# Performance work log

Hardware: AMD Instinct MI355X
Metric: run time of the kernel (lower is better)

## Reference

```python
import jax, jax.numpy as jnp
import numpy as np
import math

N_EMBD = 1024
N_HEAD = 16
N_CTX = 2048
SCALE = True
NEG = 1e10


def setup_inputs() -> dict:
    key = jax.random.key(0)
    ks = jax.random.split(key, 4)
    B, S = 2, 2048
    x = jax.random.normal(ks[0], (B, S, N_EMBD), dtype=jnp.float32)
    c_attn_w = jax.random.normal(ks[1], (N_EMBD, 3 * N_EMBD), dtype=jnp.float32) * 0.02
    c_attn_b = jnp.zeros((3 * N_EMBD,), dtype=jnp.float32)
    c_proj_w = jax.random.normal(ks[2], (N_EMBD, N_EMBD), dtype=jnp.float32) * 0.02
    c_proj_b = jnp.zeros((N_EMBD,), dtype=jnp.float32)
    return {"x": x, "c_attn_w": c_attn_w, "c_attn_b": c_attn_b,
            "c_proj_w": c_proj_w, "c_proj_b": c_proj_b}


def reference(x, c_attn_w, c_attn_b, c_proj_w, c_proj_b):
    B, S, D = x.shape
    H = N_HEAD
    hd = D // H
    qkv = x @ c_attn_w + c_attn_b                      # [B,S,3D]
    q, k, v = jnp.split(qkv, 3, axis=-1)
    # split heads -> [B,H,S,hd]
    q = q.reshape(B, S, H, hd).transpose(0, 2, 1, 3)
    k = k.reshape(B, S, H, hd).transpose(0, 2, 1, 3)
    v = v.reshape(B, S, H, hd).transpose(0, 2, 1, 3)
    w = jnp.einsum('bhqd,bhkd->bhqk', q, k)           # [B,H,S,S]
    if SCALE:
        w = w / math.sqrt(hd)
    # multiplicative causal mask trick: w*b - 1e10*(1-b)
    b = jnp.tril(jnp.ones((S, S), dtype=w.dtype))[None, None]
    w = w * b - NEG * (1.0 - b)
    w = jax.nn.softmax(w, axis=-1)
    a = jnp.einsum('bhqk,bhkd->bhqd', w, v)           # [B,H,S,hd]
    a = a.transpose(0, 2, 1, 3).reshape(B, S, D)      # merge heads
    a = a @ c_proj_w + c_proj_b
    present = jnp.stack((k, v))                       # [2,B,H,S,hd]
    return a, present
```

## Files before the change

### kernel.cpp

```cpp
#include <hip/hip_runtime.h>
#include <hip/hip_bf16.h>
#include <cstdint>
#include <cstddef>

#define SEQ 2048
#define DMODEL 1024
#define NHEAD 16
#define HDIM 64
#define MTOT 4096
#define NQKV 3072
#define KDIM 1024

#define OUT_K_BASE  4194304u
#define OUT_V_BASE  8388608u

#define QSCALE 0.18033688011112043f

typedef __attribute__((ext_vector_type(4))) float f32x4;
typedef __attribute__((ext_vector_type(8))) __bf16 bf16x8;
typedef __attribute__((ext_vector_type(8))) short s16x8;
typedef __attribute__((ext_vector_type(4))) short s16x4;
typedef __attribute__((ext_vector_type(2))) int i32x2;

static __device__ __forceinline__ unsigned short f2bf(float f) {
  unsigned int u = __builtin_bit_cast(unsigned int, f);
  u += 0x7FFFu + ((u >> 16) & 1u);
  return (unsigned short)(u >> 16);
}

static __device__ __forceinline__ float bf2f(unsigned short u) {
  unsigned int x = ((unsigned int)u) << 16;
  return __builtin_bit_cast(float, x);
}

static __device__ __forceinline__ s16x4 pack4(float4 v) {
  s16x4 r;
  r[0] = (short)f2bf(v.x);
  r[1] = (short)f2bf(v.y);
  r[2] = (short)f2bf(v.z);
  r[3] = (short)f2bf(v.w);
  return r;
}

static __device__ __forceinline__ int cvtpk(float lo, float hi) {
  int r;
  asm("v_cvt_pk_bf16_f32 %0, %1, %2" : "=v"(r) : "v"(lo), "v"(hi));
  return r;
}

static __device__ __forceinline__ f32x4 mfma16(s16x8 a, s16x8 b, f32x4 c) {
  return __builtin_amdgcn_mfma_f32_16x16x32_bf16(
      __builtin_bit_cast(bf16x8, a), __builtin_bit_cast(bf16x8, b), c, 0, 0, 0);
}

static __device__ __forceinline__ void gload16(const void* g, void* l) {
  __builtin_amdgcn_global_load_lds(
      (const __attribute__((address_space(1))) unsigned int*)(uintptr_t)g,
      (__attribute__((address_space(3))) unsigned int*)(uintptr_t)l,
      16, 0, 0);
}

#define WAITVM(n) asm volatile("s_waitcnt vmcnt(" #n ")" ::: "memory")

__global__ __launch_bounds__(256) void convert_x(
    const float* __restrict__ X, unsigned short* __restrict__ Xbf)
{
  int i = blockIdx.x * 256 + threadIdx.x;
  float4 v = reinterpret_cast<const float4*>(X)[i];
  reinterpret_cast<s16x4*>(Xbf)[i] = pack4(v);
}

__global__ __launch_bounds__(256) void convert_wt(
    const float* __restrict__ W, unsigned short* __restrict__ Wt, int N)
{
  __shared__ unsigned short t[64][72];
  const int n0 = blockIdx.x * 64, k0 = blockIdx.y * 64;
  const int tid = threadIdx.x;
#pragma unroll
  for (int i = 0; i < 4; ++i) {
    int f = tid + (i << 8);
    int r = f >> 4, c4 = (f & 15) << 2;
    float4 v = *reinterpret_cast<const float4*>(&W[(size_t)(k0 + r) * N + n0 + c4]);
    *reinterpret_cast<s16x4*>(&t[r][c4]) = pack4(v);
  }
  __syncthreads();
#pragma unroll
  for (int i = 0; i < 2; ++i) {
    int g = tid + (i << 8);
    int n = g >> 3, k8 = (g & 7) << 3;
    s16x8 o;
#pragma unroll
    for (int jj = 0; jj < 8; ++jj) o[jj] = (short)t[k8 + jj][n];
    *reinterpret_cast<s16x8*>(&Wt[(size_t)(n0 + n) * KDIM + k0 + k8]) = o;
  }
}

__global__ __launch_bounds__(256) void qkv_gemm(
    const unsigned short* __restrict__ Xbf,
    const unsigned short* __restrict__ Wt,
    const float* __restrict__ Bias,
    unsigned short* __restrict__ Qbf,
    unsigned short* __restrict__ Kbf,
    unsigned short* __restrict__ Vt,
    float* __restrict__ outp)
{
  __shared__ __align__(16) unsigned short lds_a[2][128][64];
  __shared__ __align__(16) unsigned short lds_b[2][128][64];

  const int tid = threadIdx.x;
  const int lane = tid & 63;
  const int wv = tid >> 6;
  const int wr = wv >> 1, wc = wv & 1;
  const int m0 = blockIdx.x * 128;
  const int n0 = blockIdx.y * 128;
  const int lr = lane & 15;
  const int gq = lane >> 4;

  const f32x4 fzero = {0.f, 0.f, 0.f, 0.f};
  f32x4 acc[4][4];
#pragma unroll
  for (int i = 0; i < 4; ++i)
#pragma unroll
    for (int j = 0; j < 4; ++j) acc[i][j] = fzero;

  {
    const int r0 = tid >> 3;
    const int c0 = tid & 7;
    auto stage = [&](int nb, int kk) {
#pragma unroll
      for (int i = 0; i < 4; ++i) {
        int r = r0 + (i << 5);
        int sc = ((c0 ^ (r & 7)) << 3);
        int ub = (((i << 8) + (wv << 6)) << 3);
        gload16(&Xbf[(size_t)(m0 + r) * KDIM + kk + sc], &lds_a[nb][0][0] + ub);
        gload16(&Wt[(size_t)(n0 + r) * KDIM + kk + sc], &lds_b[nb][0][0] + ub);
      }
    };
    stage(0, 0);
    stage(1, 64);
    for (int t = 0; t < 16; ++t) {
      if (t < 15) { WAITVM(8); } else { WAITVM(0); }
      __builtin_amdgcn_s_barrier();
      const int bufg = t & 1;
      __builtin_amdgcn_s_setprio(1);
#pragma unroll
      for (int kf = 0; kf < 2; ++kf) {
        s16x8 bfv[4];
#pragma unroll
        for (int ni = 0; ni < 4; ++ni) {
          int row = wc * 64 + ni * 16 + lr;
          bfv[ni] = *reinterpret_cast<const s16x8*>(
              &lds_b[bufg][row][((kf * 4 + gq) ^ (row & 7)) << 3]);
        }
#pragma unroll
        for (int mi = 0; mi < 4; ++mi) {
          int row = wr * 64 + mi * 16 + lr;
          s16x8 af = *reinterpret_cast<const s16x8*>(
              &lds_a[bufg][row][((kf * 4 + gq) ^ (row & 7)) << 3]);
#pragma unroll
          for (int ni = 0; ni < 4; ++ni)
            acc[mi][ni] = mfma16(af, bfv[ni], acc[mi][ni]);
        }
      }
      __builtin_amdgcn_s_setprio(0);
      __builtin_amdgcn_s_barrier();
      if (t < 14) stage(bufg, (t + 2) << 6);
    }
  }

  __syncthreads();
  unsigned short* T = (wv < 2) ? (&lds_a[0][0][0] + (wv << 12))
                               : (&lds_b[0][0][0] + ((wv - 2) << 12));
  const int seg = n0 >> 10;
  const int b = m0 >> 11;
  const int s0 = (m0 & 2047) + wr * 64;
  const int h = ((n0 & 1023) >> 6) + wc;
  const size_t bh = (size_t)(b * NHEAD + h);

  if (seg <= 1) {
#pragma unroll
    for (int ni = 0; ni < 4; ++ni) {
      int c = n0 + wc * 64 + ni * 16 + lr;
      float bias = Bias[c];
      int ch = 2 * ni + (lr >> 3);
      int el = lr & 7;
#pragma unroll
      for (int mi = 0; mi < 4; ++mi)
#pragma unroll
        for (int j = 0; j < 4; ++j) {
          int s_loc = mi * 16 + gq * 4 + j;
          float val = acc[mi][ni][j] + bias;
          if (seg == 0) val *= QSCALE;
          T[s_loc * 64 + ((ch ^ (s_loc & 7)) << 3) + el] = f2bf(val);
        }
    }
    unsigned short* dst = (seg == 0) ? Qbf : Kbf;
#pragma unroll
    for (int it = 0; it < 8; ++it) {
      int rr = (lane >> 3) + (it << 3);
      int cl = lane & 7;
      s16x8 vv = *reinterpret_cast<const s16x8*>(
          &T[rr * 64 + ((cl ^ (rr & 7)) << 3)]);
      size_t off = (bh * SEQ + s0 + rr) * HDIM + (cl << 3);
      *reinterpret_cast<s16x8*>(&dst[off]) = vv;
      if (seg == 1) {
        float4 lo = {bf2f((unsigned short)vv[0]), bf2f((unsigned short)vv[1]),
                     bf2f((unsigned short)vv[2]), bf2f((unsigned short)vv[3])};
        float4 hi = {bf2f((unsigned short)vv[4]), bf2f((unsigned short)vv[5]),
                     bf2f((unsigned short)vv[6]), bf2f((unsigned short)vv[7])};
        *reinterpret_cast<float4*>(&outp[OUT_K_BASE + off]) = lo;
        *reinterpret_cast<float4*>(&outp[OUT_K_BASE + off + 4]) = hi;
      }
    }
  } else {
#pragma unroll
    for (int ni = 0; ni < 4; ++ni) {
      int c = n0 + wc * 64 + ni * 16 + lr;
      float bias = Bias[c];
      int d_loc = ni * 16 + lr;
      int dsw = d_loc & 7;
#pragma unroll
      for (int mi = 0; mi < 4; ++mi)
#pragma unroll
        for (int j = 0; j < 4; ++j) {
          int s_loc = mi * 16 + gq * 4 + j;
          T[d_loc * 64 + (((s_loc >> 3) ^ dsw) << 3) + (s_loc & 7)] =
              f2bf(acc[mi][ni][j] + bias);
        }
    }
#pragma unroll
    for (int it = 0; it < 8; ++it) {
      int dl = (lane >> 3) + (it << 3);
      int cl = lane & 7;
      s16x8 vv = *reinterpret_cast<const s16x8*>(
          &T[dl * 64 + ((cl ^ (dl & 7)) << 3)]);
      *reinterpret_cast<s16x8*>(
          &Vt[(bh * HDIM + dl) * SEQ + s0 + (cl << 3)]) = vv;
    }
#pragma unroll
    for (int ni = 0; ni < 4; ++ni) {
      int c = n0 + wc * 64 + ni * 16 + lr;
      float bias = Bias[c];
      int ch = 2 * ni + (lr >> 3);
      int el = lr & 7;
#pragma unroll
      for (int mi = 0; mi < 4; ++mi)
#pragma unroll
        for (int j = 0; j < 4; ++j) {
          int s_loc = mi * 16 + gq * 4 + j;
          T[s_loc * 64 + ((ch ^ (s_loc & 7)) << 3) + el] =
              f2bf(acc[mi][ni][j] + bias);
        }
    }
#pragma unroll
    for (int it = 0; it < 8; ++it) {
      int rr = (lane >> 3) + (it << 3);
      int cl = lane & 7;
      s16x8 vv = *reinterpret_cast<const s16x8*>(
          &T[rr * 64 + ((cl ^ (rr & 7)) << 3)]);
      float4 lo = {bf2f((unsigned short)vv[0]), bf2f((unsigned short)vv[1]),
                   bf2f((unsigned short)vv[2]), bf2f((unsigned short)vv[3])};
      float4 hi = {bf2f((unsigned short)vv[4]), bf2f((unsigned short)vv[5]),
                   bf2f((unsigned short)vv[6]), bf2f((unsigned short)vv[7])};
      size_t off = (bh * SEQ + s0 + rr) * HDIM + (cl << 3);
      *reinterpret_cast<float4*>(&outp[OUT_V_BASE + off]) = lo;
      *reinterpret_cast<float4*>(&outp[OUT_V_BASE + off + 4]) = hi;
    }
  }
}

__global__ __launch_bounds__(256) void proj_gemm(
    const unsigned short* __restrict__ Abf,
    const unsigned short* __restrict__ Wpt,
    const float* __restrict__ Bias,
    float* __restrict__ out)
{
  __shared__ __align__(16) unsigned short lds_a[2][128][64];
  __shared__ __align__(16) unsigned short lds_b[2][128][64];

  const int tid = threadIdx.x;
  const int lane = tid & 63;
  const int wv = tid >> 6;
  const int wr = wv >> 1, wc = wv & 1;
  const int m0 = blockIdx.x * 128;
  const int n0 = blockIdx.y * 128;
  const int lr = lane & 15;
  const int gq = lane >> 4;

  const f32x4 fzero = {0.f, 0.f, 0.f, 0.f};
  f32x4 acc[4][4];
#pragma unroll
  for (int i = 0; i < 4; ++i)
#pragma unroll
    for (int j = 0; j < 4; ++j) acc[i][j] = fzero;

  {
    const int r0 = tid >> 3;
    const int c0 = tid & 7;
    auto stage = [&](int nb, int kk) {
#pragma unroll
      for (int i = 0; i < 4; ++i) {
        int r = r0 + (i << 5);
        int sc = ((c0 ^ (r & 7)) << 3);
        int ub = (((i << 8) + (wv << 6)) << 3);
        gload16(&Abf[(size_t)(m0 + r) * KDIM + kk + sc], &lds_a[nb][0][0] + ub);
        gload16(&Wpt[(size_t)(n0 + r) * KDIM + kk + sc], &lds_b[nb][0][0] + ub);
      }
    };
    stage(0, 0);
    stage(1, 64);
    for (int t = 0; t < 16; ++t) {
      if (t < 15) { WAITVM(8); } else { WAITVM(0); }
      __builtin_amdgcn_s_barrier();
      const int bufg = t & 1;
      __builtin_amdgcn_s_setprio(1);
#pragma unroll
      for (int kf = 0; kf < 2; ++kf) {
        s16x8 bfv[4];
#pragma unroll
        for (int ni = 0; ni < 4; ++ni) {
          int row = wc * 64 + ni * 16 + lr;
          bfv[ni] = *reinterpret_cast<const s16x8*>(
              &lds_b[bufg][row][((kf * 4 + gq) ^ (row & 7)) << 3]);
        }
#pragma unroll
        for (int mi = 0; mi < 4; ++mi) {
          int row = wr * 64 + mi * 16 + lr;
          s16x8 af = *reinterpret_cast<const s16x8*>(
              &lds_a[bufg][row][((kf * 4 + gq) ^ (row & 7)) << 3]);
#pragma unroll
          for (int ni = 0; ni < 4; ++ni)
            acc[mi][ni] = mfma16(af, bfv[ni], acc[mi][ni]);
        }
      }
      __builtin_amdgcn_s_setprio(0);
      __builtin_amdgcn_s_barrier();
      if (t < 14) stage(bufg, (t + 2) << 6);
    }
  }

#pragma unroll
  for (int ni = 0; ni < 4; ++ni) {
    int c = n0 + wc * 64 + ni * 16 + lr;
    float bias = Bias[c];
#pragma unroll
    for (int mi = 0; mi < 4; ++mi) {
#pragma unroll
      for (int j = 0; j < 4; ++j) {
        int m = m0 + wr * 64 + mi * 16 + gq * 4 + j;
        out[(size_t)m * DMODEL + c] = acc[mi][ni][j] + bias;
      }
    }
  }
}

__global__ __launch_bounds__(256, 4) void attn_fwd(
    const unsigned short* __restrict__ Qbf,
    const unsigned short* __restrict__ Kbf,
    const unsigned short* __restrict__ Vtg,
    unsigned short* __restrict__ Abf)
{
  __shared__ __align__(16) unsigned short K_lds[2][64][64];
  __shared__ __align__(16) unsigned short V_lds[2][64][64];
  __shared__ __align__(16) unsigned short P_lds[4][16][64];

  const int tid = threadIdx.x;
  const int lane = tid & 63;
  const int wv = tid >> 6;
  const int bid = blockIdx.x;
  const int qt = 31 - (bid >> 5);
  const int bh = bid & 31;

  const int lr = lane & 15;
  const int gq = lane >> 4;

  const unsigned short* Kg = Kbf + (size_t)bh * (SEQ * HDIM);
  const unsigned short* Vg = Vtg + (size_t)bh * (SEQ * HDIM);
  const unsigned short* Qg = Qbf + (size_t)bh * (SEQ * HDIM)
                                 + (size_t)(qt * 64 + wv * 16) * HDIM;

  s16x8 qf0 = *reinterpret_cast<const s16x8*>(&Qg[lr * 64 + (gq << 3)]);
  s16x8 qf1 = *reinterpret_cast<const s16x8*>(&Qg[lr * 64 + 32 + (gq << 3)]);

  const f32x4 fzero = {0.f, 0.f, 0.f, 0.f};
  f32x4 O[4];
  float mrow = -1e30f, lrow = 0.f;
#pragma unroll
  for (int no = 0; no < 4; ++no) O[no] = fzero;

#define STAGE(kv0, nb)                                                        \
  {                                                                           \
    _Pragma("unroll")                                                         \
    for (int i = 0; i < 2; ++i) {                                             \
      int L = tid + (i << 8);                                                 \
      int r = L >> 3, c = L & 7;                                              \
      int cc = (c ^ (r & 7)) << 3;                                            \
      int ubase = ((i << 8) + (wv << 6)) << 3;                                \
      gload16(&Kg[(((kv0) + r) << 6) + cc], &K_lds[nb][0][0] + ubase);        \
      gload16(&Vg[((size_t)r << 11) + (kv0) + cc], &V_lds[nb][0][0] + ubase); \
    }                                                                         \
  }

  STAGE(0, 0);

  for (int t = 0; t <= qt; ++t) {
    __syncthreads();
    if (t < qt) STAGE((t + 1) * 64, (t + 1) & 1);
    const int buf = t & 1;

    f32x4 sc[4];
#pragma unroll
    for (int ni = 0; ni < 4; ++ni) {
      int kr = ni * 16 + lr;
      int sw = kr & 7;
      s16x8 kb0 = *reinterpret_cast<const s16x8*>(&K_lds[buf][kr][(gq ^ sw) << 3]);
      s16x8 kb1 = *reinterpret_cast<const s16x8*>(&K_lds[buf][kr][((gq + 4) ^ sw) << 3]);
      f32x4 tacc = mfma16(kb0, qf0, fzero);
      sc[ni] = mfma16(kb1, qf1, tacc);
    }

    if (t == qt) {
      int qloc = wv * 16 + lr;
#pragma unroll
      for (int ni = 0; ni < 4; ++ni)
#pragma unroll
        for (int r = 0; r < 4; ++r)
          if (ni * 16 + gq * 4 + r > qloc) sc[ni][r] = -1e30f;
    }

    float tmax = fmaxf(fmaxf(fmaxf(sc[0][0], sc[0][1]), fmaxf(sc[0][2], sc[0][3])),
                       fmaxf(fmaxf(sc[1][0], sc[1][1]), fmaxf(sc[1][2], sc[1][3])));
    tmax = fmaxf(tmax,
                 fmaxf(fmaxf(fmaxf(sc[2][0], sc[2][1]), fmaxf(sc[2][2], sc[2][3])),
                       fmaxf(fmaxf(sc[3][0], sc[3][1]), fmaxf(sc[3][2], sc[3][3]))));
    tmax = fmaxf(tmax, __shfl_xor(tmax, 16));
    tmax = fmaxf(tmax, __shfl_xor(tmax, 32));
    float newm = fmaxf(mrow, tmax);
    float fs = __builtin_amdgcn_exp2f(mrow - newm);
    mrow = newm;
    float rs = 0.f;
#pragma unroll
    for (int ni = 0; ni < 4; ++ni) {
#pragma unroll
      for (int r = 0; r < 4; ++r) {
        float p = __builtin_amdgcn_exp2f(sc[ni][r] - newm);
        sc[ni][r] = p;
        rs += p;
      }
    }
    rs += __shfl_xor(rs, 16);
    rs += __shfl_xor(rs, 32);
    lrow = lrow * fs + rs;
#pragma unroll
    for (int no = 0; no < 4; ++no) O[no] *= fs;

    {
      unsigned short* Prow = &P_lds[wv][lr][0];
      const int swl = lr & 7;
#pragma unroll
      for (int ni = 0; ni < 4; ++ni) {
        i32x2 d2;
        d2[0] = cvtpk(sc[ni][0], sc[ni][1]);
        d2[1] = cvtpk(sc[ni][2], sc[ni][3]);
        int off = ((((2 * ni) + (gq >> 1)) ^ swl) << 3) + ((gq & 1) << 2);
        *reinterpret_cast<i32x2*>(&Prow[off]) = d2;
      }
      s16x8 pB0 = *reinterpret_cast<const s16x8*>(&Prow[(gq ^ swl) << 3]);
      s16x8 pB1 = *reinterpret_cast<const s16x8*>(&Prow[((gq + 4) ^ swl) << 3]);

#pragma unroll
      for (int no = 0; no < 4; ++no) {
        int dr = no * 16 + lr;
        int sw = dr & 7;
        s16x8 vb0 = *reinterpret_cast<const s16x8*>(&V_lds[buf][dr][(gq ^ sw) << 3]);
        s16x8 vb1 = *reinterpret_cast<const s16x8*>(&V_lds[buf][dr][((gq + 4) ^ sw) << 3]);
        O[no] = mfma16(vb0, pB0, O[no]);
        O[no] = mfma16(vb1, pB1, O[no]);
      }
    }
  }

  const int b = bh >> 4, h = bh & 15;
  float inv = 1.0f / lrow;
  int srow = qt * 64 + wv * 16 + lr;
  size_t base = (size_t)(b * SEQ + srow) * DMODEL + h * 64 + (gq << 2);
#pragma unroll
  for (int no = 0; no < 4; ++no) {
    s16x4 ov;
#pragma unroll
    for (int r = 0; r < 4; ++r) ov[r] = (short)f2bf(O[no][r] * inv);
    *reinterpret_cast<s16x4*>(&Abf[base + no * 16]) = ov;
  }
#undef STAGE
}

extern "C" void kernel_launch(void* const* d_in, const int* in_sizes, int n_in,
                              void* d_out, int out_size, void* d_ws, size_t ws_size,
                              hipStream_t stream) {
  const float* x        = (const float*)d_in[0];
  const float* c_attn_w = (const float*)d_in[1];
  const float* c_attn_b = (const float*)d_in[2];
  const float* c_proj_w = (const float*)d_in[3];
  const float* c_proj_b = (const float*)d_in[4];
  float* out = (float*)d_out;

  unsigned short* Qbf = (unsigned short*)d_ws;
  unsigned short* Xbf = Qbf + 4194304;
  unsigned short* Abf = Xbf;
  unsigned short* Wt  = Qbf + 8388608;
  unsigned short* Wpt = Wt;
  unsigned short* Kbf = (unsigned short*)out;
  unsigned short* Vt  = Kbf + 4194304;

  convert_x<<<dim3(4096), 256, 0, stream>>>(x, Xbf);
  convert_wt<<<dim3(48, 16), 256, 0, stream>>>(c_attn_w, Wt, NQKV);
  qkv_gemm<<<dim3(32, 24), 256, 0, stream>>>(Xbf, Wt, c_attn_b, Qbf, Kbf, Vt, out);
  convert_wt<<<dim3(16, 16), 256, 0, stream>>>(c_proj_w, Wpt, DMODEL);
  attn_fwd<<<dim3(1024), 256, 0, stream>>>(Qbf, Kbf, Vt, Abf);
  proj_gemm<<<dim3(32, 8), 256, 0, stream>>>(Abf, Wpt, c_proj_b, out);
}
```

Before: 113.5 us.

## Load QKV GEMM B operand directly from global into registers, dropping B LDS

The QKV projection GEMM no longer stages the weight tile through shared memory. Each wave loads its B fragments straight from global memory into double-buffered registers one k-step ahead, while A keeps the LDS double buffer. This halves LDS usage and LDS read traffic, which could raise occupancy. The costs are more global load instructions per wave (B rows are read redundantly by the two waves sharing a column), more registers, and a changed wait/barrier schedule.

```diff
diff --git a/kernel.cpp b/kernel.cpp
--- a/kernel.cpp
+++ b/kernel.cpp
@@ -105,7 +105,6 @@
     float* __restrict__ outp)
 {
   __shared__ __align__(16) unsigned short lds_a[2][128][64];
-  __shared__ __align__(16) unsigned short lds_b[2][128][64];
 
   const int tid = threadIdx.x;
   const int lane = tid & 63;
@@ -126,51 +125,68 @@
   {
     const int r0 = tid >> 3;
     const int c0 = tid & 7;
-    auto stage = [&](int nb, int kk) {
+    auto stageA = [&](int nb, int kk) {
 #pragma unroll
       for (int i = 0; i < 4; ++i) {
         int r = r0 + (i << 5);
         int sc = ((c0 ^ (r & 7)) << 3);
         int ub = (((i << 8) + (wv << 6)) << 3);
         gload16(&Xbf[(size_t)(m0 + r) * KDIM + kk + sc], &lds_a[nb][0][0] + ub);
-        gload16(&Wt[(size_t)(n0 + r) * KDIM + kk + sc], &lds_b[nb][0][0] + ub);
       }
     };
-    stage(0, 0);
-    stage(1, 64);
-    for (int t = 0; t < 16; ++t) {
-      if (t < 15) { WAITVM(8); } else { WAITVM(0); }
-      __builtin_amdgcn_s_barrier();
-      const int bufg = t & 1;
-      __builtin_amdgcn_s_setprio(1);
-#pragma unroll
-      for (int kf = 0; kf < 2; ++kf) {
-        s16x8 bfv[4];
-#pragma unroll
-        for (int ni = 0; ni < 4; ++ni) {
-          int row = wc * 64 + ni * 16 + lr;
-          bfv[ni] = *reinterpret_cast<const s16x8*>(
-              &lds_b[bufg][row][((kf * 4 + gq) ^ (row & 7)) << 3]);
-        }
-#pragma unroll
-        for (int mi = 0; mi < 4; ++mi) {
-          int row = wr * 64 + mi * 16 + lr;
-          s16x8 af = *reinterpret_cast<const s16x8*>(
-              &lds_a[bufg][row][((kf * 4 + gq) ^ (row & 7)) << 3]);
-#pragma unroll
-          for (int ni = 0; ni < 4; ++ni)
-            acc[mi][ni] = mfma16(af, bfv[ni], acc[mi][ni]);
-        }
-      }
-      __builtin_amdgcn_s_setprio(0);
-      __builtin_amdgcn_s_barrier();
-      if (t < 14) stage(bufg, (t + 2) << 6);
-    }
+    const unsigned short* Bbase =
+        &Wt[(size_t)(n0 + wc * 64 + lr) * KDIM + (gq << 3)];
+    auto loadB = [&](s16x8* dst, int kk) {
+#pragma unroll
+      for (int kf = 0; kf < 2; ++kf)
+#pragma unroll
+        for (int ni = 0; ni < 4; ++ni)
+          dst[kf * 4 + ni] = *reinterpret_cast<const s16x8*>(
+              Bbase + (size_t)ni * (16 * KDIM) + kk + kf * 32);
+    };
+
+    s16x8 bA[8], bB[8];
+    stageA(0, 0);
+    stageA(1, 64);
+    loadB(bA, 0);
+    WAITVM(0);
+    __builtin_amdgcn_s_barrier();
+
+#define QKV_STEP(T, bcur, bnxt)                                               \
+    {                                                                         \
+      if ((T) < 15) loadB(bnxt, ((T) + 1) << 6);                              \
+      const int bufg = (T) & 1;                                               \
+      __builtin_amdgcn_s_setprio(1);                                          \
+      _Pragma("unroll")                                                       \
+      for (int kf = 0; kf < 2; ++kf) {                                        \
+        _Pragma("unroll")                                                     \
+        for (int mi = 0; mi < 4; ++mi) {                                      \
+          int row = wr * 64 + mi * 16 + lr;                                   \
+          s16x8 af = *reinterpret_cast<const s16x8*>(                         \
+              &lds_a[bufg][row][((kf * 4 + gq) ^ (row & 7)) << 3]);           \
+          _Pragma("unroll")                                                   \
+          for (int ni = 0; ni < 4; ++ni)                                      \
+            acc[mi][ni] = mfma16(af, (bcur)[kf * 4 + ni], acc[mi][ni]);       \
+        }                                                                     \
+      }                                                                       \
+      __builtin_amdgcn_s_setprio(0);                                         \
+      __builtin_amdgcn_s_barrier();                                          \
+      if ((T) < 14) stageA(bufg, ((T) + 2) << 6);                            \
+      if ((T) < 14)      { WAITVM(4); }                                       \
+      else if ((T) == 14){ WAITVM(0); }                                       \
+      __builtin_amdgcn_s_barrier();                                          \
+    }
+
+#pragma unroll
+    for (int tt = 0; tt < 8; ++tt) {
+      QKV_STEP(2 * tt,     bA, bB);
+      QKV_STEP(2 * tt + 1, bB, bA);
+    }
+#undef QKV_STEP
   }
 
   __syncthreads();
-  unsigned short* T = (wv < 2) ? (&lds_a[0][0][0] + (wv << 12))
-                               : (&lds_b[0][0][0] + ((wv - 2) << 12));
+  unsigned short* T = &lds_a[0][0][0] + (wv << 12);
   const int seg = n0 >> 10;
   const int b = m0 >> 11;
   const int s0 = (m0 & 2047) + wr * 64;
```

New measurement: 138.0 us. 21.6% more time.
